# Optimization experiments

Measured on AMD Instinct MI355X. Metric: run time of the kernel, lower is better.

## Reference

```python
import jax, jax.numpy as jnp
import numpy as np

N = 200000
CIN = 64
COUT = 64
K = 9           # taps in a 1x3x3 or 3x1x3 kernel
EPS = 1e-5      # BatchNorm1d eps
SLOPE = 0.01    # LeakyReLU default negative slope


def setup_inputs() -> dict:
    key = jax.random.key(0)
    ks = jax.random.split(key, 7)
    scale = 0.05
    return {
        "x": jax.random.normal(ks[0], (N, CIN), dtype=jnp.float32),
        "w_a0": jax.random.normal(ks[1], (K, CIN, COUT), dtype=jnp.float32) * scale,
        "gamma_a0": jnp.ones((COUT,), jnp.float32),
        "beta_a0": jnp.zeros((COUT,), jnp.float32),
        "w_a1": jax.random.normal(ks[2], (K, COUT, COUT), dtype=jnp.float32) * scale,
        "gamma_a1": jnp.ones((COUT,), jnp.float32),
        "beta_a1": jnp.zeros((COUT,), jnp.float32),
        "w_b0": jax.random.normal(ks[3], (K, CIN, COUT), dtype=jnp.float32) * scale,
        "gamma_b0": jnp.ones((COUT,), jnp.float32),
        "beta_b0": jnp.zeros((COUT,), jnp.float32),
        "w_b1": jax.random.normal(ks[4], (K, COUT, COUT), dtype=jnp.float32) * scale,
        "gamma_b1": jnp.ones((COUT,), jnp.float32),
        "beta_b1": jnp.zeros((COUT,), jnp.float32),
        "idx_133": jax.random.randint(ks[5], (N, K), 0, N),
        "idx_313": jax.random.randint(ks[6], (N, K), 0, N),
    }


def subm_conv(feat, idx, w):
    # gather [N,K,Cin] -> GEMM with [K,Cin,Cout] -> [N,Cout]
    gathered = feat[idx]
    return jnp.einsum('nkc,kcd->nd', gathered, w)


def bn_train(feat, gamma, beta):
    # BatchNorm1d (training mode): biased batch statistics over N
    mean = jnp.mean(feat, axis=0)
    var = jnp.var(feat, axis=0)
    return (feat - mean) * jax.lax.rsqrt(var + EPS) * gamma + beta


def lrelu(feat):
    return jnp.where(feat >= 0, feat, SLOPE * feat)


def reference(x, w_a0, gamma_a0, beta_a0, w_a1, gamma_a1, beta_a1,
              w_b0, gamma_b0, beta_b0, w_b1, gamma_b1, beta_b1,
              idx_133, idx_313):
    # A branch: 1x3x3 -> act -> bn -> 3x1x3 -> act -> bn
    A = subm_conv(x, idx_133, w_a0)
    A = bn_train(lrelu(A), gamma_a0, beta_a0)
    A = subm_conv(A, idx_313, w_a1)
    A = bn_train(lrelu(A), gamma_a1, beta_a1)
    # B0 branch is computed but unused in the original (B = conv_B1(A))
    B0 = bn_train(lrelu(subm_conv(x, idx_313, w_b0)), gamma_b0, beta_b0)  # noqa: F841 (dead, DCE'd)
    # B branch actually uses A per original source
    B = subm_conv(A, idx_133, w_b1)
    B = bn_train(lrelu(B), gamma_b1, beta_b1)
    return A + B
```

## Files before the change

### kernel.cpp

```cpp
#include <hip/hip_runtime.h>

#define N_ROWS 200000
#define NTAP 9
#define BM 128
#define NBLK 1563
#define WSTRIDE 584
#define WCHUNKS 73
#define WT_ELEMS (64*WSTRIDE)
#define TAB_ELEMS ((size_t)N_ROWS*64)
#define VEC8_CNT 1600000

using bf16x8 = __attribute__((ext_vector_type(8))) __bf16;
using f32x4  = __attribute__((ext_vector_type(4))) float;

__device__ __forceinline__ float b2f(unsigned short u) {
  unsigned int x = ((unsigned int)u) << 16;
  return __builtin_bit_cast(float, x);
}
__device__ __forceinline__ unsigned short f2b(float f) {
  unsigned int x = __builtin_bit_cast(unsigned int, f);
  x = x + 0x7fffu + ((x >> 16) & 1u);
  return (unsigned short)(x >> 16);
}
__device__ __forceinline__ void async16(const void* g, void* l) {
  __builtin_amdgcn_global_load_lds((const __attribute__((address_space(1))) unsigned int*)g,
                                   (__attribute__((address_space(3))) unsigned int*)l,
                                   16, 0, 0);
}

__global__ void transp_idx(const int* __restrict__ src, int* __restrict__ dst) {
  int i = blockIdx.x * 256 + threadIdx.x;
  if (i >= N_ROWS * NTAP) return;
  int n = i / NTAP, t = i - n * NTAP;
  dst[t * N_ROWS + n] = src[i];
}

__global__ void prep_x(const float* __restrict__ x, unsigned short* __restrict__ T) {
  int i = blockIdx.x * 256 + threadIdx.x;
  if (i >= VEC8_CNT) return;
  const float4* xv = (const float4*)x + (size_t)i * 2;
  float4 a = xv[0], b = xv[1];
  uint4 o;
  o.x = (unsigned)f2b(a.x) | ((unsigned)f2b(a.y) << 16);
  o.y = (unsigned)f2b(a.z) | ((unsigned)f2b(a.w) << 16);
  o.z = (unsigned)f2b(b.x) | ((unsigned)f2b(b.y) << 16);
  o.w = (unsigned)f2b(b.z) | ((unsigned)f2b(b.w) << 16);
  ((uint4*)T)[i] = o;
}

__global__ void prep_ws(const float* __restrict__ w, const float* __restrict__ stats,
                        unsigned short* __restrict__ wt) {
  int i = blockIdx.x * 256 + threadIdx.x;
  if (i >= WT_ELEMS) return;
  int n = i / WSTRIDE, k = i - n * WSTRIDE;
  float v = 0.f;
  if (k < 576) {
    int tap = k >> 6, ci = k & 63;
    float s = stats ? stats[ci] : 1.0f;
    v = w[tap * 4096 + ci * 64 + n] * s;
  }
  wt[i] = f2b(v);
}

__global__ void prep_bias(const float* __restrict__ w, const float* __restrict__ stats,
                          float* __restrict__ bias) {
  int co = threadIdx.x & 63, part = threadIdx.x >> 6;
  float s = 0.f;
#pragma unroll 4
  for (int e = part; e < 576; e += 4) {
    int tap = e >> 6, ci = e & 63;
    s += stats[64 + ci] * w[tap * 4096 + ci * 64 + co];
  }
  __shared__ float r[4][64];
  r[part][co] = s;
  __syncthreads();
  if (part == 0) bias[co] = r[0][co] + r[1][co] + r[2][co] + r[3][co];
}

__global__ __launch_bounds__(512, 4) void conv_k(
    const unsigned short* __restrict__ T,
    const int* __restrict__ idxT,
    const unsigned short* __restrict__ Wt,
    const float* __restrict__ bias,
    unsigned short* __restrict__ L,
    float* __restrict__ partials)
{
  __shared__ unsigned short Wlds[64][WSTRIDE];
  __shared__ float psum[8][2][64];

  const int tid = threadIdx.x;
  const int w = tid >> 6;
  const int l = tid & 63;
  const int blk = blockIdx.x;
  const int rowbase = blk * BM;
  const int kgrp = l >> 4;

  for (int c = w; c < WCHUNKS; c += 8)
    async16(Wt + c * 512 + l * 8, (unsigned short*)&Wlds[0][0] + c * 512);

  int mrow = rowbase + w * 16 + (l & 15);
  if (mrow > N_ROWS - 1) mrow = N_ROWS - 1;

  int ix[NTAP];
#pragma unroll
  for (int t = 0; t < NTAP; ++t) ix[t] = idxT[t * N_ROWS + mrow];

  float binit[4] = {0.f, 0.f, 0.f, 0.f};
  if (bias) {
#pragma unroll
    for (int f = 0; f < 4; ++f) binit[f] = bias[f * 16 + (l & 15)];
  }

  __syncthreads();

  const char* Tb = (const char*)T;
  bf16x8 A0[NTAP], A1[NTAP];
#pragma unroll
  for (int t = 0; t < NTAP; ++t) {
    const char* p = Tb + (size_t)((unsigned)ix[t] * 128u) + kgrp * 16;
    A0[t] = *(const bf16x8*)p;
    A1[t] = *(const bf16x8*)(p + 64);
  }
  __builtin_amdgcn_sched_barrier(0);

  f32x4 acc[4];
#pragma unroll
  for (int f = 0; f < 4; ++f) acc[f] = (f32x4){binit[f], binit[f], binit[f], binit[f]};

#pragma unroll
  for (int t = 0; t < NTAP; ++t) {
    const unsigned short* wb = &Wlds[l & 15][t * 64 + kgrp * 8];
#pragma unroll
    for (int f = 0; f < 4; ++f) {
      bf16x8 b0 = *(const bf16x8*)(wb + f * 16 * WSTRIDE);
      bf16x8 b1 = *(const bf16x8*)(wb + f * 16 * WSTRIDE + 32);
      acc[f] = __builtin_amdgcn_mfma_f32_16x16x32_bf16(A0[t], b0, acc[f], 0, 0, 0);
      acc[f] = __builtin_amdgcn_mfma_f32_16x16x32_bf16(A1[t], b1, acc[f], 0, 0, 0);
    }
  }

#pragma unroll
  for (int f = 0; f < 4; ++f) {
    int c = f * 16 + (l & 15);
    float sm = 0.f, sq = 0.f;
#pragma unroll
    for (int j = 0; j < 4; ++j) {
      int gr = rowbase + w * 16 + kgrp * 4 + j;
      float v = acc[f][j];
      float y = v >= 0.f ? v : 0.01f * v;
      if (gr < N_ROWS) {
        L[(size_t)gr * 64 + c] = f2b(y);
        sm += y; sq += y * y;
      }
    }
    sm += __shfl_xor(sm, 16); sm += __shfl_xor(sm, 32);
    sq += __shfl_xor(sq, 16); sq += __shfl_xor(sq, 32);
    if (l < 16) { psum[w][0][c] = sm; psum[w][1][c] = sq; }
  }
  __syncthreads();
  if (tid < 128) {
    int j = tid >> 6, c = tid & 63;
    float tot = 0.f;
#pragma unroll
    for (int ww = 0; ww < 8; ++ww) tot += psum[ww][j][c];
    partials[(size_t)(j * 64 + c) * NBLK + blk] = tot;
  }
}

__global__ void reduce_k(const float* __restrict__ part, const float* __restrict__ gamma,
                         const float* __restrict__ beta, float* __restrict__ stats) {
  int c = blockIdx.x, t = threadIdx.x;
  float s = 0.f, q = 0.f;
  for (int b = t; b < NBLK; b += 256) {
    s += part[(size_t)c * NBLK + b];
    q += part[(size_t)(64 + c) * NBLK + b];
  }
#pragma unroll
  for (int m = 1; m < 64; m <<= 1) { s += __shfl_xor(s, m); q += __shfl_xor(q, m); }
  __shared__ float rs[4], rq[4];
  if ((t & 63) == 0) { rs[t >> 6] = s; rq[t >> 6] = q; }
  __syncthreads();
  if (t == 0) {
    float su = rs[0] + rs[1] + rs[2] + rs[3];
    float qu = rq[0] + rq[1] + rq[2] + rq[3];
    float mean = su / (float)N_ROWS;
    float var = qu / (float)N_ROWS - mean * mean;
    float r = rsqrtf(var + 1e-5f);
    float sc = gamma[c] * r;
    stats[c] = sc;
    stats[64 + c] = beta[c] - mean * sc;
  }
}

__global__ void final_k(const unsigned short* __restrict__ L2v,
                        const unsigned short* __restrict__ L3v,
                        const float* __restrict__ st2, const float* __restrict__ st3,
                        float* __restrict__ out) {
  int i = blockIdx.x * 256 + threadIdx.x;
  if (i >= VEC8_CNT) return;
  uint4 av = ((const uint4*)L2v)[i];
  uint4 yv = ((const uint4*)L3v)[i];
  int c0 = (i & 7) * 8;
  unsigned va[4] = {av.x, av.y, av.z, av.w};
  unsigned vy[4] = {yv.x, yv.y, yv.z, yv.w};
  float o[8];
#pragma unroll
  for (int h = 0; h < 4; ++h) {
    int c = c0 + 2 * h;
    float a0 = b2f((unsigned short)(va[h] & 0xffff));
    float a1 = b2f((unsigned short)(va[h] >> 16));
    float y0 = b2f((unsigned short)(vy[h] & 0xffff));
    float y1 = b2f((unsigned short)(vy[h] >> 16));
    o[2 * h]     = a0 * st2[c]     + st2[64 + c]     + y0 * st3[c]     + st3[64 + c];
    o[2 * h + 1] = a1 * st2[c + 1] + st2[64 + c + 1] + y1 * st3[c + 1] + st3[64 + c + 1];
  }
  float4* ov = (float4*)(out + (size_t)i * 8);
  ov[0] = make_float4(o[0], o[1], o[2], o[3]);
  ov[1] = make_float4(o[4], o[5], o[6], o[7]);
}

extern "C" void kernel_launch(void* const* d_in, const int* in_sizes, int n_in,
                              void* d_out, int out_size, void* d_ws, size_t ws_size,
                              hipStream_t stream) {
  (void)in_sizes; (void)n_in; (void)out_size; (void)ws_size;
  const float* x    = (const float*)d_in[0];
  const float* w_a0 = (const float*)d_in[1];
  const float* g_a0 = (const float*)d_in[2];
  const float* b_a0 = (const float*)d_in[3];
  const float* w_a1 = (const float*)d_in[4];
  const float* g_a1 = (const float*)d_in[5];
  const float* b_a1 = (const float*)d_in[6];
  const float* w_b1 = (const float*)d_in[10];
  const float* g_b1 = (const float*)d_in[11];
  const float* b_b1 = (const float*)d_in[12];
  const int* idx133 = (const int*)d_in[13];
  const int* idx313 = (const int*)d_in[14];
  float* out = (float*)d_out;

  char* ws = (char*)d_ws;
  unsigned short* wt0 = (unsigned short*)ws;
  unsigned short* wt1 = wt0 + WT_ELEMS;
  unsigned short* wt2 = wt1 + WT_ELEMS;
  unsigned short* Tx  = wt2 + WT_ELEMS;
  unsigned short* L1  = Tx + TAB_ELEMS;
  unsigned short* L2  = L1 + TAB_ELEMS;
  unsigned short* L3  = Tx;
  int* it133 = (int*)(L2 + TAB_ELEMS);
  int* it313 = it133 + N_ROWS * NTAP;
  float* part = (float*)(it313 + N_ROWS * NTAP);
  float* st1 = part + 2 * 64 * NBLK;
  float* st2 = st1 + 128;
  float* st3 = st2 + 128;
  float* bias1 = st3 + 128;
  float* bias2 = bias1 + 64;

  transp_idx<<<(N_ROWS * NTAP + 255) / 256, 256, 0, stream>>>(idx133, it133);
  transp_idx<<<(N_ROWS * NTAP + 255) / 256, 256, 0, stream>>>(idx313, it313);
  prep_x<<<(VEC8_CNT + 255) / 256, 256, 0, stream>>>(x, Tx);
  prep_ws<<<(WT_ELEMS + 255) / 256, 256, 0, stream>>>(w_a0, nullptr, wt0);

  conv_k<<<NBLK, 512, 0, stream>>>(Tx, it133, wt0, nullptr, L1, part);
  reduce_k<<<64, 256, 0, stream>>>(part, g_a0, b_a0, st1);
  prep_ws<<<(WT_ELEMS + 255) / 256, 256, 0, stream>>>(w_a1, st1, wt1);
  prep_bias<<<1, 256, 0, stream>>>(w_a1, st1, bias1);

  conv_k<<<NBLK, 512, 0, stream>>>(L1, it313, wt1, bias1, L2, part);
  reduce_k<<<64, 256, 0, stream>>>(part, g_a1, b_a1, st2);
  prep_ws<<<(WT_ELEMS + 255) / 256, 256, 0, stream>>>(w_b1, st2, wt2);
  prep_bias<<<1, 256, 0, stream>>>(w_b1, st2, bias2);

  conv_k<<<NBLK, 512, 0, stream>>>(L2, it133, wt2, bias2, L3, part);
  reduce_k<<<64, 256, 0, stream>>>(part, g_b1, b_b1, st3);

  final_k<<<(VEC8_CNT + 255) / 256, 256, 0, stream>>>(L2, L3, st2, st3, out);
}
```

Baseline: 220.3 us.

## Stream conv weights through double-buffered LDS chunks to raise occupancy

The full 9-tap weight tile is no longer held in LDS. It is split into three 3-tap chunks held in a two-slot buffer (about 51KB instead of about 75KB). The third chunk is loaded asynchronously while the second chunk's MFMAs run, and the BN partial-sum scratch reuses the weight buffer. Launch bounds rise to allow more resident blocks, so more waves can hide the random-gather latency. The cost is extra barriers per block, three weight fetches per block from L2, and a possible bank-conflict change from the new 200-element stride.

```diff
diff --git a/kernel.cpp b/kernel.cpp
--- a/kernel.cpp
+++ b/kernel.cpp
@@ -4,9 +4,9 @@
 #define NTAP 9
 #define BM 128
 #define NBLK 1563
-#define WSTRIDE 584
-#define WCHUNKS 73
-#define WT_ELEMS (64*WSTRIDE)
+#define CSTRIDE 200
+#define CHUNK_ELEMS (64*CSTRIDE)
+#define WT_ELEMS (3*CHUNK_ELEMS)
 #define TAB_ELEMS ((size_t)N_ROWS*64)
 #define VEC8_CNT 1600000
 
@@ -52,12 +52,14 @@
                         unsigned short* __restrict__ wt) {
   int i = blockIdx.x * 256 + threadIdx.x;
   if (i >= WT_ELEMS) return;
-  int n = i / WSTRIDE, k = i - n * WSTRIDE;
+  int chunk = i / CHUNK_ELEMS;
+  int r = (i / CSTRIDE) & 63;
+  int k = i % CSTRIDE;
   float v = 0.f;
-  if (k < 576) {
-    int tap = k >> 6, ci = k & 63;
+  if (k < 192) {
+    int tap = chunk * 3 + (k >> 6), ci = k & 63;
     float s = stats ? stats[ci] : 1.0f;
-    v = w[tap * 4096 + ci * 64 + n] * s;
+    v = w[tap * 4096 + ci * 64 + r] * s;
   }
   wt[i] = f2b(v);
 }
@@ -77,7 +79,7 @@
   if (part == 0) bias[co] = r[0][co] + r[1][co] + r[2][co] + r[3][co];
 }
 
-__global__ __launch_bounds__(512, 4) void conv_k(
+__global__ __launch_bounds__(512, 6) void conv_k(
     const unsigned short* __restrict__ T,
     const int* __restrict__ idxT,
     const unsigned short* __restrict__ Wt,
@@ -85,8 +87,7 @@
     unsigned short* __restrict__ L,
     float* __restrict__ partials)
 {
-  __shared__ unsigned short Wlds[64][WSTRIDE];
-  __shared__ float psum[8][2][64];
+  __shared__ unsigned short Wlds[2][64][CSTRIDE];
 
   const int tid = threadIdx.x;
   const int w = tid >> 6;
@@ -95,8 +96,10 @@
   const int rowbase = blk * BM;
   const int kgrp = l >> 4;
 
-  for (int c = w; c < WCHUNKS; c += 8)
-    async16(Wt + c * 512 + l * 8, (unsigned short*)&Wlds[0][0] + c * 512);
+  for (int v = tid; v < 1600; v += 512) {
+    async16(Wt + v * 8, (unsigned short*)&Wlds[0][0][0] + v * 8);
+    async16(Wt + CHUNK_ELEMS + v * 8, (unsigned short*)&Wlds[1][0][0] + v * 8);
+  }
 
   int mrow = rowbase + w * 16 + (l & 15);
   if (mrow > N_ROWS - 1) mrow = N_ROWS - 1;
@@ -110,8 +113,6 @@
 #pragma unroll
     for (int f = 0; f < 4; ++f) binit[f] = bias[f * 16 + (l & 15)];
   }
-
-  __syncthreads();
 
   const char* Tb = (const char*)T;
   bf16x8 A0[NTAP], A1[NTAP];
@@ -121,24 +122,40 @@
     A0[t] = *(const bf16x8*)p;
     A1[t] = *(const bf16x8*)(p + 64);
   }
-  __builtin_amdgcn_sched_barrier(0);
+
+  __syncthreads();
 
   f32x4 acc[4];
 #pragma unroll
   for (int f = 0; f < 4; ++f) acc[f] = (f32x4){binit[f], binit[f], binit[f], binit[f]};
 
-#pragma unroll
-  for (int t = 0; t < NTAP; ++t) {
-    const unsigned short* wb = &Wlds[l & 15][t * 64 + kgrp * 8];
-#pragma unroll
-    for (int f = 0; f < 4; ++f) {
-      bf16x8 b0 = *(const bf16x8*)(wb + f * 16 * WSTRIDE);
-      bf16x8 b1 = *(const bf16x8*)(wb + f * 16 * WSTRIDE + 32);
-      acc[f] = __builtin_amdgcn_mfma_f32_16x16x32_bf16(A0[t], b0, acc[f], 0, 0, 0);
-      acc[f] = __builtin_amdgcn_mfma_f32_16x16x32_bf16(A1[t], b1, acc[f], 0, 0, 0);
-    }
-  }
-
+#define MFMA_GROUP(buf, tbase)                                                  \
+  {                                                                             \
+    _Pragma("unroll")                                                           \
+    for (int lt = 0; lt < 3; ++lt) {                                            \
+      int t = (tbase) + lt;                                                     \
+      const unsigned short* wb = &Wlds[buf][l & 15][lt * 64 + kgrp * 8];        \
+      _Pragma("unroll")                                                         \
+      for (int f = 0; f < 4; ++f) {                                             \
+        bf16x8 b0 = *(const bf16x8*)(wb + f * 16 * CSTRIDE);                    \
+        bf16x8 b1 = *(const bf16x8*)(wb + f * 16 * CSTRIDE + 32);               \
+        acc[f] = __builtin_amdgcn_mfma_f32_16x16x32_bf16(A0[t], b0, acc[f], 0, 0, 0); \
+        acc[f] = __builtin_amdgcn_mfma_f32_16x16x32_bf16(A1[t], b1, acc[f], 0, 0, 0); \
+      }                                                                         \
+    }                                                                           \
+  }
+
+  MFMA_GROUP(0, 0)
+  __syncthreads();
+  for (int v = tid; v < 1600; v += 512)
+    async16(Wt + 2 * CHUNK_ELEMS + v * 8, (unsigned short*)&Wlds[0][0][0] + v * 8);
+  MFMA_GROUP(1, 3)
+  __syncthreads();
+  MFMA_GROUP(2 & 0, 6)
+  __syncthreads();
+#undef MFMA_GROUP
+
+  float* psum = (float*)&Wlds[0][0][0];
 #pragma unroll
   for (int f = 0; f < 4; ++f) {
     int c = f * 16 + (l & 15);
@@ -155,14 +172,14 @@
     }
     sm += __shfl_xor(sm, 16); sm += __shfl_xor(sm, 32);
     sq += __shfl_xor(sq, 16); sq += __shfl_xor(sq, 32);
-    if (l < 16) { psum[w][0][c] = sm; psum[w][1][c] = sq; }
+    if (l < 16) { psum[(w * 2 + 0) * 64 + c] = sm; psum[(w * 2 + 1) * 64 + c] = sq; }
   }
   __syncthreads();
   if (tid < 128) {
     int j = tid >> 6, c = tid & 63;
     float tot = 0.f;
 #pragma unroll
-    for (int ww = 0; ww < 8; ++ww) tot += psum[ww][j][c];
+    for (int ww = 0; ww < 8; ++ww) tot += psum[(ww * 2 + j) * 64 + c];
     partials[(size_t)(j * 64 + c) * NBLK + blk] = tot;
   }
 }
```

New measurement: 292.7 us. 32.9% more time.
